# Kernel optimization log

Measured on AMD Instinct MI355X. Metric: run time of the kernel, lower is better.

Reference implementation:

```python
import jax, jax.numpy as jnp
import numpy as np

B, S, D, H, DK, DV = 4, 2048, 1024, 16, 64, 64

def setup_inputs() -> dict:
    key = jax.random.key(0)
    ks = jax.random.split(key, 7)
    scale = 0.02
    queries = jax.random.normal(ks[0], (B, S, D), jnp.float32)
    keys_ = jax.random.normal(ks[1], (B, S, D), jnp.float32)
    values = jax.random.normal(ks[2], (B, S, D), jnp.float32)
    # causal mask: 1 where attendable, 0 where masked
    mask = jnp.tril(jnp.ones((S, S), jnp.int32))[None, None, :, :]
    W_Q = jax.random.normal(ks[3], (D, H * DK), jnp.float32) * scale
    W_K = jax.random.normal(ks[4], (D, H * DK), jnp.float32) * scale
    W_V = jax.random.normal(ks[5], (D, H * DV), jnp.float32) * scale
    W_O = jax.random.normal(ks[6], (H * DV, D), jnp.float32) * scale
    return {"queries": queries, "keys": keys_, "values": values, "mask": mask,
            "W_Q": W_Q, "W_K": W_K, "W_V": W_V, "W_O": W_O}

def reference(queries, keys, values, mask, W_Q, W_K, W_V, W_O):
    b, skv, _ = keys.shape
    sq = queries.shape[1]
    scaling = 1.0 / (DK ** 0.5)
    Q = (queries @ W_Q).reshape(b, sq, H, DK)   # [B,Sq,H,DK]
    K = (keys @ W_K).reshape(b, skv, H, DK)     # [B,Skv,H,DK]
    V = (values @ W_V).reshape(b, skv, H, DV)   # [B,Skv,H,DV]
    scores = jnp.einsum('bqhd,bkhd->bhqk', Q, K)
    scores = jnp.where(mask == 0, -jnp.inf, scores)
    probs = jax.nn.softmax(scores * scaling, axis=-1)
    attn = jnp.einsum('bhqk,bkhd->bqhd', probs, V).reshape(b, sq, H * DV)
    return attn @ W_O
```

## Files before the change

kernel.cpp:

```cpp
#include <hip/hip_runtime.h>
#include <hip/hip_bf16.h>


typedef __attribute__((ext_vector_type(8))) __bf16 bf16x8;
typedef __attribute__((ext_vector_type(8))) unsigned short ushort8v;
typedef __attribute__((ext_vector_type(4))) unsigned short ushort4v;
typedef __attribute__((ext_vector_type(4))) unsigned uint4v;
typedef __attribute__((ext_vector_type(2))) unsigned uint2v;
typedef __attribute__((ext_vector_type(4))) float float4v;

#define MFMA16(a, b, c) __builtin_amdgcn_mfma_f32_16x16x32_bf16((a), (b), (c), 0, 0, 0)
#define GLDS16(g, l)                                                     \
    __builtin_amdgcn_global_load_lds(                                    \
        (const __attribute__((address_space(1))) void*)(g),              \
        (__attribute__((address_space(3))) void*)(l), 16, 0, 0)

__device__ __forceinline__ unsigned short f2bf(float f) {
    union { float f; unsigned u; } v; v.f = f;
    unsigned r = v.u + 0x7fffu + ((v.u >> 16) & 1u);
    return (unsigned short)(r >> 16);
}
__device__ __forceinline__ unsigned pkbf(float a, float b) {
    union { float f; unsigned u; } x, y; x.f = a; y.f = b;
    return __builtin_amdgcn_perm(y.u + 0x8000u, x.u + 0x8000u, 0x07060302u);
}
__device__ __forceinline__ float exp2_fast(float x) {
#if __has_builtin(__builtin_amdgcn_exp2f)
    return __builtin_amdgcn_exp2f(x);
#else
    return __builtin_exp2f(x);
#endif
}

__global__ __launch_bounds__(256) void transpose_w4(
    const float* __restrict__ W0, const float* __restrict__ W1,
    const float* __restrict__ W2, const float* __restrict__ W3,
    unsigned short* __restrict__ T0, unsigned short* __restrict__ T1,
    unsigned short* __restrict__ T2, unsigned short* __restrict__ T3)
{
    __shared__ unsigned short T[64][72];
    const int z = blockIdx.z;
    const float* W = z == 0 ? W0 : z == 1 ? W1 : z == 2 ? W2 : W3;
    unsigned short* Wt = z == 0 ? T0 : z == 1 ? T1 : z == 2 ? T2 : T3;
    const float scale = (z == 1) ? 0.125f * 1.44269504088896f : 1.0f;
    const int t = threadIdx.x;
    const int n0 = blockIdx.x * 64, k0 = blockIdx.y * 64;
    for (int i = 0; i < 4; i++) {
        int idx = i * 256 + t, r = idx >> 4, c = (idx & 15) * 4;
        float4v v = *(const float4v*)&W[(size_t)(k0 + r) * 1024 + n0 + c];
        T[c + 0][r] = f2bf(v.x * scale); T[c + 1][r] = f2bf(v.y * scale);
        T[c + 2][r] = f2bf(v.z * scale); T[c + 3][r] = f2bf(v.w * scale);
    }
    __syncthreads();
    for (int i = 0; i < 4; i++) {
        int idx = i * 256 + t, r = idx >> 4, c = (idx & 15) * 4;
        ushort4v o; o.x = T[r][c]; o.y = T[r][c + 1]; o.z = T[r][c + 2]; o.w = T[r][c + 3];
        *(ushort4v*)&Wt[(size_t)(n0 + r) * 1024 + k0 + c] = o;
    }
}

__global__ __launch_bounds__(256) void qkv_gemm(
    const float* __restrict__ Aq, const float* __restrict__ Ak,
    const float* __restrict__ Av,
    const unsigned short* __restrict__ WQt, const unsigned short* __restrict__ WKt,
    const unsigned short* __restrict__ WVt,
    unsigned short* __restrict__ Qb, unsigned short* __restrict__ Kb,
    unsigned short* __restrict__ Vto)
{
    __shared__ unsigned short As[128 * 64];
    __shared__ unsigned short Bs[128 * 64];

    const int t = threadIdx.x;
    const int lane = t & 63, w = t >> 6;
    const int lanelo = lane & 15, quad = lane >> 4;
    const int wm = w >> 1, wn = w & 1;

    const int d = blockIdx.x;
    const int xcd = d & 7;
    const int s = d >> 3;
    const int group = s >> 6;
    const int u = s & 63;
    const bool vsw = (group == 2);

    const float* act; const unsigned short* wt; unsigned short* out;
    if (group == 0)      { act = Aq; wt = WQt; out = Qb; }
    else if (group == 1) { act = Ak; wt = WKt; out = Kb; }
    else                 { act = Av; wt = WVt; out = Vto; }

    const int big = (((u >> 3) << 3) | xcd) * 128;
    const int sml = (u & 7) * 128;
    int m0, n0, ldc;
    if (!vsw) { m0 = big; n0 = sml; ldc = 1024; }
    else      { n0 = big; m0 = sml; ldc = 8192; }
    const int act0 = vsw ? n0 : m0;
    const int wt0  = vsw ? m0 : n0;
    unsigned short* actS = vsw ? Bs : As;
    unsigned short* wtS  = vsw ? As : Bs;

    float4v acc[4][4];
    for (int i = 0; i < 4; i++)
        for (int j = 0; j < 4; j++) acc[i][j] = (float4v)(0.f);

    for (int k0 = 0; k0 < 1024; k0 += 64) {
        for (int i = 0; i < 4; i++) {
            int idx = i * 256 + t, row = idx >> 3, ch = idx & 7;
            GLDS16(wt + (size_t)(wt0 + row) * 1024 + k0 + ch * 8, &wtS[idx * 8]);
        }
        for (int i = 0; i < 4; i++) {
            int si = i * 256 + t, row = si >> 3, ch = si & 7;
            const float* ap = act + (size_t)(act0 + row) * 1024 + k0 + ch * 8;
            float4v x = *(const float4v*)ap;
            float4v y = *(const float4v*)(ap + 4);
            uint4v o4 = { pkbf(x.x, x.y), pkbf(x.z, x.w),
                          pkbf(y.x, y.y), pkbf(y.z, y.w) };
            *(uint4v*)&actS[row * 64 + ch * 8] = o4;
        }
        __syncthreads();
        for (int ks = 0; ks < 2; ks++) {
            bf16x8 af[4], bfr[4];
            for (int mi = 0; mi < 4; mi++)
                af[mi] = *(const bf16x8*)&As[(wm * 64 + mi * 16 + lanelo) * 64 + ks * 32 + quad * 8];
            for (int ni = 0; ni < 4; ni++)
                bfr[ni] = *(const bf16x8*)&Bs[(wn * 64 + ni * 16 + lanelo) * 64 + ks * 32 + quad * 8];
            for (int mi = 0; mi < 4; mi++)
                for (int ni = 0; ni < 4; ni++)
                    acc[mi][ni] = MFMA16(af[mi], bfr[ni], acc[mi][ni]);
        }
        __syncthreads();
    }

    for (int mi = 0; mi < 4; mi++)
        for (int ni = 0; ni < 4; ni++) {
            int col = n0 + wn * 64 + ni * 16 + lanelo;
            for (int rr = 0; rr < 4; rr++) {
                int row = m0 + wm * 64 + mi * 16 + quad * 4 + rr;
                out[(size_t)row * ldc + col] = f2bf(acc[mi][ni][rr]);
            }
        }
}

__global__ __launch_bounds__(256) void gemm_bb(
    const unsigned short* __restrict__ A, const unsigned short* __restrict__ Bt,
    float* __restrict__ Cp, int M, int N, int K)
{
    __shared__ unsigned short As[128 * 64];
    __shared__ unsigned short Bs[128 * 64];

    const int t = threadIdx.x;
    const int lane = t & 63, w = t >> 6;
    const int lanelo = lane & 15, quad = lane >> 4;
    const int wm = w >> 1, wn = w & 1;

    const int d = blockIdx.x;
    const int xcd = d & 7, s = d >> 3;
    const int m0 = ((((s >> 3) << 3) | xcd)) * 128;
    const int n0 = (s & 7) * 128;

    float4v acc[4][4];
    for (int i = 0; i < 4; i++)
        for (int j = 0; j < 4; j++) acc[i][j] = (float4v)(0.f);

    for (int k0 = 0; k0 < K; k0 += 64) {
        for (int i = 0; i < 4; i++) {
            int idx = i * 256 + t, row = idx >> 3, ch = idx & 7;
            GLDS16(A + (size_t)(m0 + row) * K + k0 + ch * 8, &As[idx * 8]);
        }
        for (int i = 0; i < 4; i++) {
            int idx = i * 256 + t, row = idx >> 3, ch = idx & 7;
            GLDS16(Bt + (size_t)(n0 + row) * K + k0 + ch * 8, &Bs[idx * 8]);
        }
        __syncthreads();
        for (int ks = 0; ks < 2; ks++) {
            bf16x8 af[4], bfr[4];
            for (int mi = 0; mi < 4; mi++)
                af[mi] = *(const bf16x8*)&As[(wm * 64 + mi * 16 + lanelo) * 64 + ks * 32 + quad * 8];
            for (int ni = 0; ni < 4; ni++)
                bfr[ni] = *(const bf16x8*)&Bs[(wn * 64 + ni * 16 + lanelo) * 64 + ks * 32 + quad * 8];
            for (int mi = 0; mi < 4; mi++)
                for (int ni = 0; ni < 4; ni++)
                    acc[mi][ni] = MFMA16(af[mi], bfr[ni], acc[mi][ni]);
        }
        __syncthreads();
    }

    for (int mi = 0; mi < 4; mi++)
        for (int ni = 0; ni < 4; ni++) {
            int col = n0 + wn * 64 + ni * 16 + lanelo;
            for (int r = 0; r < 4; r++) {
                int row = m0 + wm * 64 + mi * 16 + quad * 4 + r;
                Cp[(size_t)row * N + col] = acc[mi][ni][r];
            }
        }
}

__global__ __launch_bounds__(256, 4) void attn_k(
    const unsigned short* __restrict__ Qb, const unsigned short* __restrict__ Kb,
    const unsigned short* __restrict__ Vt, unsigned short* __restrict__ Ob)
{
    __shared__ __align__(16) unsigned short Ks[2][64 * 64];
    __shared__ __align__(16) unsigned short Vs[2][64 * 64];
    __shared__ __align__(16) unsigned short Ps[4][16 * 64];

    const int t = threadIdx.x;
    const int lane = t & 63, w = t >> 6;
    const int lanelo = lane & 15, quad = lane >> 4;
    const int bh = blockIdx.x;
    const int b = bh >> 4, h = bh & 15;

    unsigned short* pw = &Ps[w][0];
    const int rsw = (lanelo & 7) * 8;
    const int l7 = lanelo & 7;

    auto stage = [&](int buf, int kt) {
        for (int i = 0; i < 2; i++) {
            int idx = i * 256 + t, row = idx >> 3, ch = idx & 7;
            GLDS16(Kb + ((size_t)(b * 2048 + kt * 64 + row)) * 1024 + h * 64
                       + ((ch ^ (row & 7)) << 3),
                   &Ks[buf][idx * 8]);
        }
        for (int i = 0; i < 2; i++) {
            int idx = i * 256 + t, row = idx >> 3, ch = idx & 7;
            GLDS16(Vt + (size_t)(h * 64 + row) * 8192 + b * 2048 + kt * 64
                       + ((ch ^ (row & 7)) << 3),
                   &Vs[buf][idx * 8]);
        }
    };

    for (int half = 0; half < 2; half++) {
        const int qt = half ? blockIdx.y : 31 - blockIdx.y;
        const int qb = qt * 64;
        const int nkt = qt + 1;
        const int q = qb + w * 16 + lanelo;

        bf16x8 qf[2];
        {
            const unsigned short* qp = Qb + ((size_t)(b * 2048) + q) * 1024 + h * 64 + quad * 8;
            qf[0] = *(const bf16x8*)(qp);
            qf[1] = *(const bf16x8*)(qp + 32);
        }
        float4v o[4];
        for (int i = 0; i < 4; i++) o[i] = (float4v)(0.f);
        float m_ = -__builtin_inff(), l_ = 0.f;

        stage(0, 0);
        __syncthreads();

        int cur = 0;
        for (int kt = 0; kt < nkt; kt++) {
            if (kt + 1 < nkt) stage(cur ^ 1, kt + 1);

            const unsigned short* ks = &Ks[cur][0];
            const unsigned short* vs = &Vs[cur][0];

            float4v sc[4];
            for (int nt = 0; nt < 4; nt++) {
                sc[nt] = (float4v)(0.f);
                for (int c = 0; c < 2; c++) {
                    bf16x8 kf = *(const bf16x8*)
                        &ks[(nt * 16 + lanelo) * 64 + ((c * 32 + quad * 8) ^ rsw)];
                    sc[nt] = MFMA16(kf, qf[c], sc[nt]);
                }
            }
            if (kt == nkt - 1) {
                const int kb0 = qb + quad * 4;
                for (int nt = 0; nt < 4; nt++)
                    for (int r = 0; r < 4; r++)
                        if (kb0 + nt * 16 + r > q) sc[nt][r] = -__builtin_inff();
            }
            float mx = sc[0][0];
            for (int nt = 0; nt < 4; nt++)
                for (int r = 0; r < 4; r++) mx = fmaxf(mx, sc[nt][r]);
            mx = fmaxf(mx, __shfl_xor(mx, 16, 64));
            mx = fmaxf(mx, __shfl_xor(mx, 32, 64));
            if (!__all(mx <= m_ + 8.f)) {
                float mnew = fmaxf(m_, mx);
                float alpha = exp2_fast(m_ - mnew);
                l_ *= alpha;
                for (int vt = 0; vt < 4; vt++)
                    for (int r = 0; r < 4; r++) o[vt][r] *= alpha;
                m_ = mnew;
            }
            float rs = 0.f;
            for (int nt = 0; nt < 4; nt++)
                for (int r = 0; r < 4; r++) {
                    float e = exp2_fast(sc[nt][r] - m_);
                    sc[nt][r] = e; rs += e;
                }
            rs += __shfl_xor(rs, 16, 64);
            rs += __shfl_xor(rs, 32, 64);
            l_ += rs;

            for (int nt = 0; nt < 4; nt++) {
                uint2v pv;
                pv.x = pkbf(sc[nt][0], sc[nt][1]);
                pv.y = pkbf(sc[nt][2], sc[nt][3]);
                *(uint2v*)((char*)pw + lanelo * 128
                           + ((((nt << 1) | (quad >> 1)) ^ l7) << 4)
                           + ((quad & 1) << 3)) = pv;
            }
            asm volatile("s_waitcnt lgkmcnt(0)" ::: "memory");
            __builtin_amdgcn_sched_barrier(0);
            for (int c = 0; c < 2; c++) {
                bf16x8 pf = *(const bf16x8*)((const char*)pw + lanelo * 128
                                             + (((c * 4 + quad) ^ l7) << 4));
                for (int vt = 0; vt < 4; vt++) {
                    bf16x8 vf = *(const bf16x8*)
                        &vs[(vt * 16 + lanelo) * 64 + ((c * 32 + quad * 8) ^ rsw)];
                    o[vt] = MFMA16(vf, pf, o[vt]);
                }
            }
            __syncthreads();
            cur ^= 1;
        }

        float inv = 1.0f / l_;
        for (int vt = 0; vt < 4; vt++) {
            uint2v ov;
            ov.x = pkbf(o[vt][0] * inv, o[vt][1] * inv);
            ov.y = pkbf(o[vt][2] * inv, o[vt][3] * inv);
            *(uint2v*)((char*)pw + lanelo * 128
                       + ((((vt << 1) | (quad >> 1)) ^ l7) << 4)
                       + ((quad & 1) << 3)) = ov;
        }
        asm volatile("s_waitcnt lgkmcnt(0)" ::: "memory");
        __builtin_amdgcn_sched_barrier(0);
        for (int i = 0; i < 2; i++) {
            int qr = i * 8 + (lane >> 3);
            int ch = lane & 7;
            ushort8v ov = *(const ushort8v*)((const char*)pw + qr * 128
                                             + ((ch ^ (qr & 7)) << 4));
            *(ushort8v*)(Ob + ((size_t)(b * 2048) + qb + w * 16 + qr) * 1024
                         + h * 64 + ch * 8) = ov;
        }
    }
}

extern "C" void kernel_launch(void* const* d_in, const int* in_sizes, int n_in,
                              void* d_out, int out_size, void* d_ws, size_t ws_size,
                              hipStream_t stream) {
    const float* queries = (const float*)d_in[0];
    const float* keys    = (const float*)d_in[1];
    const float* values  = (const float*)d_in[2];
    const float* W_Q = (const float*)d_in[4];
    const float* W_K = (const float*)d_in[5];
    const float* W_V = (const float*)d_in[6];
    const float* W_O = (const float*)d_in[7];

    const size_t SZ = (size_t)4 * 2048 * 1024;
    const size_t WSZ = (size_t)1024 * 1024;
    unsigned short* Qb  = (unsigned short*)d_ws;
    unsigned short* Kb  = Qb + SZ;
    unsigned short* Vt  = Kb + SZ;
    unsigned short* Ab  = Vt + SZ;
    unsigned short* WQt = Ab + SZ;
    unsigned short* WKt = WQt + WSZ;
    unsigned short* WVt = WKt + WSZ;
    unsigned short* WOt = WVt + WSZ;

    dim3 blk(256);
    hipLaunchKernelGGL(transpose_w4, dim3(16, 16, 4), blk, 0, stream,
                       W_Q, W_K, W_V, W_O, WQt, WKt, WVt, WOt);

    hipLaunchKernelGGL(qkv_gemm, dim3(1536), blk, 0, stream,
                       queries, keys, values, WQt, WKt, WVt, Qb, Kb, Vt);

    hipLaunchKernelGGL(attn_k, dim3(64, 16), blk, 0, stream, Qb, Kb, Vt, Ab);

    hipLaunchKernelGGL(gemm_bb, dim3(512), blk, 0, stream,
                       Ab, WOt, (float*)d_out, 8192, 1024, 1024);
}
```

Baseline: 336.3 us.

## Double-buffer LDS tiles in QKV and output GEMMs to overlap loads with MFMA

Both projection GEMM kernels now use two LDS buffers per operand. The next K-tile's global-to-LDS loads (and, in the QKV kernel, the fp32 activation register loads) are issued before the current tile's MFMAs, and the converted activations are written to the other buffer afterwards. This hides global memory latency behind compute and removes one barrier per iteration. In exchange, LDS use doubles to 64KB per block, which may lower occupancy, and the prefetched activations cost extra registers.

New measurement: 383.3 us. 14.0% more time.

```diff
diff --git a/kernel.cpp b/kernel.cpp
--- a/kernel.cpp
+++ b/kernel.cpp
@@ -67,8 +67,8 @@
     unsigned short* __restrict__ Qb, unsigned short* __restrict__ Kb,
     unsigned short* __restrict__ Vto)
 {
-    __shared__ unsigned short As[128 * 64];
-    __shared__ unsigned short Bs[128 * 64];
+    __shared__ __align__(16) unsigned short wtS[2][128 * 64];
+    __shared__ __align__(16) unsigned short actS[2][128 * 64];
 
     const int t = threadIdx.x;
     const int lane = t & 63, w = t >> 6;
@@ -94,38 +94,60 @@
     else      { n0 = big; m0 = sml; ldc = 8192; }
     const int act0 = vsw ? n0 : m0;
     const int wt0  = vsw ? m0 : n0;
-    unsigned short* actS = vsw ? Bs : As;
-    unsigned short* wtS  = vsw ? As : Bs;
+
+    float4v ar[4][2];
+
+    auto wt_stage = [&](int buf, int k0) {
+        for (int i = 0; i < 4; i++) {
+            int idx = i * 256 + t, row = idx >> 3, ch = idx & 7;
+            GLDS16(wt + (size_t)(wt0 + row) * 1024 + k0 + ch * 8, &wtS[buf][idx * 8]);
+        }
+    };
+    auto act_load = [&](int k0) {
+        for (int i = 0; i < 4; i++) {
+            int si = i * 256 + t, row = si >> 3, ch = si & 7;
+            const float* ap = act + (size_t)(act0 + row) * 1024 + k0 + ch * 8;
+            ar[i][0] = *(const float4v*)ap;
+            ar[i][1] = *(const float4v*)(ap + 4);
+        }
+    };
+    auto act_write = [&](int buf) {
+        for (int i = 0; i < 4; i++) {
+            int si = i * 256 + t;
+            uint4v o4 = { pkbf(ar[i][0].x, ar[i][0].y), pkbf(ar[i][0].z, ar[i][0].w),
+                          pkbf(ar[i][1].x, ar[i][1].y), pkbf(ar[i][1].z, ar[i][1].w) };
+            *(uint4v*)&actS[buf][si * 8] = o4;
+        }
+    };
 
     float4v acc[4][4];
     for (int i = 0; i < 4; i++)
         for (int j = 0; j < 4; j++) acc[i][j] = (float4v)(0.f);
 
-    for (int k0 = 0; k0 < 1024; k0 += 64) {
-        for (int i = 0; i < 4; i++) {
-            int idx = i * 256 + t, row = idx >> 3, ch = idx & 7;
-            GLDS16(wt + (size_t)(wt0 + row) * 1024 + k0 + ch * 8, &wtS[idx * 8]);
-        }
-        for (int i = 0; i < 4; i++) {
-            int si = i * 256 + t, row = si >> 3, ch = si & 7;
-            const float* ap = act + (size_t)(act0 + row) * 1024 + k0 + ch * 8;
-            float4v x = *(const float4v*)ap;
-            float4v y = *(const float4v*)(ap + 4);
-            uint4v o4 = { pkbf(x.x, x.y), pkbf(x.z, x.w),
-                          pkbf(y.x, y.y), pkbf(y.z, y.w) };
-            *(uint4v*)&actS[row * 64 + ch * 8] = o4;
-        }
-        __syncthreads();
+    wt_stage(0, 0);
+    act_load(0);
+    act_write(0);
+    __syncthreads();
+
+    for (int tt = 0; tt < 16; ++tt) {
+        const int cur = tt & 1;
+        if (tt < 15) {
+            wt_stage(cur ^ 1, (tt + 1) * 64);
+            act_load((tt + 1) * 64);
+        }
+        const unsigned short* As_ = vsw ? &wtS[cur][0] : &actS[cur][0];
+        const unsigned short* Bs_ = vsw ? &actS[cur][0] : &wtS[cur][0];
         for (int ks = 0; ks < 2; ks++) {
             bf16x8 af[4], bfr[4];
             for (int mi = 0; mi < 4; mi++)
-                af[mi] = *(const bf16x8*)&As[(wm * 64 + mi * 16 + lanelo) * 64 + ks * 32 + quad * 8];
+                af[mi] = *(const bf16x8*)&As_[(wm * 64 + mi * 16 + lanelo) * 64 + ks * 32 + quad * 8];
             for (int ni = 0; ni < 4; ni++)
-                bfr[ni] = *(const bf16x8*)&Bs[(wn * 64 + ni * 16 + lanelo) * 64 + ks * 32 + quad * 8];
+                bfr[ni] = *(const bf16x8*)&Bs_[(wn * 64 + ni * 16 + lanelo) * 64 + ks * 32 + quad * 8];
             for (int mi = 0; mi < 4; mi++)
                 for (int ni = 0; ni < 4; ni++)
                     acc[mi][ni] = MFMA16(af[mi], bfr[ni], acc[mi][ni]);
         }
+        if (tt < 15) act_write(cur ^ 1);
         __syncthreads();
     }
 
@@ -143,8 +165,8 @@
     const unsigned short* __restrict__ A, const unsigned short* __restrict__ Bt,
     float* __restrict__ Cp, int M, int N, int K)
 {
-    __shared__ unsigned short As[128 * 64];
-    __shared__ unsigned short Bs[128 * 64];
+    __shared__ __align__(16) unsigned short As[2][128 * 64];
+    __shared__ __align__(16) unsigned short Bs[2][128 * 64];
 
     const int t = threadIdx.x;
     const int lane = t & 63, w = t >> 6;
@@ -156,26 +178,34 @@
     const int m0 = ((((s >> 3) << 3) | xcd)) * 128;
     const int n0 = (s & 7) * 128;
 
+    auto stage = [&](int buf, int k0) {
+        for (int i = 0; i < 4; i++) {
+            int idx = i * 256 + t, row = idx >> 3, ch = idx & 7;
+            GLDS16(A + (size_t)(m0 + row) * K + k0 + ch * 8, &As[buf][idx * 8]);
+        }
+        for (int i = 0; i < 4; i++) {
+            int idx = i * 256 + t, row = idx >> 3, ch = idx & 7;
+            GLDS16(Bt + (size_t)(n0 + row) * K + k0 + ch * 8, &Bs[buf][idx * 8]);
+        }
+    };
+
     float4v acc[4][4];
     for (int i = 0; i < 4; i++)
         for (int j = 0; j < 4; j++) acc[i][j] = (float4v)(0.f);
 
-    for (int k0 = 0; k0 < K; k0 += 64) {
-        for (int i = 0; i < 4; i++) {
-            int idx = i * 256 + t, row = idx >> 3, ch = idx & 7;
-            GLDS16(A + (size_t)(m0 + row) * K + k0 + ch * 8, &As[idx * 8]);
-        }
-        for (int i = 0; i < 4; i++) {
-            int idx = i * 256 + t, row = idx >> 3, ch = idx & 7;
-            GLDS16(Bt + (size_t)(n0 + row) * K + k0 + ch * 8, &Bs[idx * 8]);
-        }
-        __syncthreads();
+    const int NT = K >> 6;
+    stage(0, 0);
+    __syncthreads();
+
+    for (int tt = 0; tt < NT; ++tt) {
+        const int cur = tt & 1;
+        if (tt + 1 < NT) stage(cur ^ 1, (tt + 1) * 64);
         for (int ks = 0; ks < 2; ks++) {
             bf16x8 af[4], bfr[4];
             for (int mi = 0; mi < 4; mi++)
-                af[mi] = *(const bf16x8*)&As[(wm * 64 + mi * 16 + lanelo) * 64 + ks * 32 + quad * 8];
+                af[mi] = *(const bf16x8*)&As[cur][(wm * 64 + mi * 16 + lanelo) * 64 + ks * 32 + quad * 8];
             for (int ni = 0; ni < 4; ni++)
-                bfr[ni] = *(const bf16x8*)&Bs[(wn * 64 + ni * 16 + lanelo) * 64 + ks * 32 + quad * 8];
+                bfr[ni] = *(const bf16x8*)&Bs[cur][(wn * 64 + ni * 16 + lanelo) * 64 + ks * 32 + quad * 8];
             for (int mi = 0; mi < 4; mi++)
                 for (int ni = 0; ni < 4; ni++)
                     acc[mi][ni] = MFMA16(af[mi], bfr[ni], acc[mi][ni]);
```
